# Optimization experiments

Hardware: AMD Instinct MI355X
Metric: run time of the kernel (lower is better)

## Reference

```python
import jax, jax.numpy as jnp
import numpy as np

N_HEADS = 16
HEAD_SIZE = 64
D_EMBD = 1024
BLOCK_SIZE = 1024
B, T = 4, 1024


def setup_inputs() -> dict:
    key = jax.random.key(0)
    ks = jax.random.split(key, 6)
    s = 0.02
    x = jax.random.normal(ks[0], (B, T, D_EMBD), dtype=jnp.float32)
    # per-head bias-free Q/K/V projections, stacked: [H, C, Hs]
    Wq = jax.random.normal(ks[1], (N_HEADS, D_EMBD, HEAD_SIZE), dtype=jnp.float32) * s
    Wk = jax.random.normal(ks[2], (N_HEADS, D_EMBD, HEAD_SIZE), dtype=jnp.float32) * s
    Wv = jax.random.normal(ks[3], (N_HEADS, D_EMBD, HEAD_SIZE), dtype=jnp.float32) * s
    # output projection W_o: Linear(d_embd, d_embd) with bias
    Wo = jax.random.normal(ks[4], (D_EMBD, D_EMBD), dtype=jnp.float32) * s
    bo = jax.random.normal(ks[5], (D_EMBD,), dtype=jnp.float32) * s
    return {"x": x, "Wq": Wq, "Wk": Wk, "Wv": Wv, "Wo": Wo, "bo": bo}


def reference(x, Wq, Wk, Wv, Wo, bo):
    # Batched equivalent of the per-head loop: q,k,v: [B, H, T, Hs]
    q = jnp.einsum('btc,hcs->bhts', x, Wq)
    k = jnp.einsum('btc,hcs->bhts', x, Wk)
    v = jnp.einsum('btc,hcs->bhts', x, Wv)
    scale = 1.0 / jnp.sqrt(jnp.asarray(HEAD_SIZE, dtype=x.dtype))
    scores = jnp.einsum('bhts,bhus->bhtu', q, k) * scale  # [B,H,T,T]
    causal = jnp.tril(jnp.ones((T, T), dtype=bool))
    scores = jnp.where(causal[None, None, :, :], scores, jnp.asarray(-jnp.inf, dtype=x.dtype))
    wei = jax.nn.softmax(scores, axis=-1)  # dropout p=0.0 -> identity
    out = jnp.einsum('bhtu,bhus->bhts', wei, v)  # [B,H,T,Hs]
    out = out.transpose(0, 2, 1, 3).reshape(B, T, D_EMBD)  # concat heads
    return out @ Wo.T + bo  # final Linear; dropout p=0.0 -> identity
```

## Files before the change

kernel.cpp:

```cpp
#include <hip/hip_runtime.h>
#include <hip/hip_bf16.h>
#include <math.h>

#define NH 16
#define HS 64
#define DE 1024
#define TT 1024
#define BBATCH 4
#define MTOK 4096

typedef __bf16 v8bf __attribute__((ext_vector_type(8)));
typedef __bf16 v4bf __attribute__((ext_vector_type(4)));
typedef float  v4f  __attribute__((ext_vector_type(4)));

__device__ __forceinline__ void gl_lds16(const __bf16* g, __bf16* l) {
    __builtin_amdgcn_global_load_lds(
        (const __attribute__((address_space(1))) unsigned int*)g,
        (__attribute__((address_space(3))) unsigned int*)l, 16, 0, 0);
}

__global__ __launch_bounds__(256) void prep_all_kernel(
    const float* __restrict__ x,  __bf16* __restrict__ xb,
    const float* __restrict__ Wo, __bf16* __restrict__ Wob,
    const float* __restrict__ Wq, const float* __restrict__ Wk,
    const float* __restrict__ Wv, __bf16* __restrict__ Wt)
{
    const int bid = blockIdx.x;
    const int t = threadIdx.x;
    if (bid < 5120) {
        int i = bid * 256 + t;
        const float* in; __bf16* out;
        if (i < 1048576) { in = x;  out = xb; }
        else             { in = Wo; out = Wob; i -= 1048576; }
        float4 v = ((const float4*)in)[i];
        v4bf o;
        o[0] = (__bf16)v.x; o[1] = (__bf16)v.y; o[2] = (__bf16)v.z; o[3] = (__bf16)v.w;
        *(v4bf*)&out[(size_t)i * 4] = o;
        return;
    }
    const int bid2 = bid - 5120;
    const int c0 = (bid2 & 15) * 64, h = (bid2 >> 4) & 15, m = bid2 >> 8;
    const float* W = (m == 0) ? Wq : (m == 1) ? Wk : Wv;
    __shared__ float tile[64][65];
    #pragma unroll
    for (int pp = 0; pp < 16; ++pp) {
        int cl = pp * 4 + (t >> 6);
        int s  = t & 63;
        tile[cl][s] = W[((size_t)h * DE + c0 + cl) * HS + s];
    }
    __syncthreads();
    #pragma unroll
    for (int pp = 0; pp < 16; ++pp) {
        int s  = pp * 4 + (t >> 6);
        int cl = t & 63;
        Wt[((size_t)(m * DE + h * HS + s)) * DE + c0 + cl] = (__bf16)tile[cl][s];
    }
}

__device__ __forceinline__ void gemm_stage(
    const __bf16* __restrict__ Ab, const __bf16* __restrict__ Bb,
    __bf16* As, __bf16* Bs, int K, int k0, int w, int l)
{
    #pragma unroll
    for (int i = 0; i < 4; ++i) {
        int p   = i * 256 + w * 64 + l;
        int row = p >> 3;
        int lc  = (p & 7) ^ (row & 7);
        gl_lds16(Ab + (size_t)row * K + k0 + lc * 8, As + p * 8);
        gl_lds16(Bb + (size_t)row * K + k0 + lc * 8, Bs + p * 8);
    }
}

__global__ __launch_bounds__(256) void gemm_bt_kernel(
    const __bf16* __restrict__ A, const __bf16* __restrict__ Bt,
    int K, int mode,
    __bf16* __restrict__ qk_out, __bf16* __restrict__ vt_out,
    float* __restrict__ f_out, const float* __restrict__ bias)
{
    __shared__ __align__(16) __bf16 As[2][128 * 64];
    __shared__ __align__(16) __bf16 Bs[2][128 * 64];
    const int tid = threadIdx.x;
    const int w = tid >> 6, l = tid & 63;
    const int wm = w >> 1, wn = w & 1;
    const int lhi = l >> 4, llo = l & 15;
    const int sw0 = ((lhi ^ (llo & 7)) << 3);
    const int sw1 = sw0 ^ 32;

    const int lin = blockIdx.x;
    const int xcd = lin & 7, j = lin >> 3;
    const int bm = xcd * 4 + (j & 3);
    const int bn = j >> 2;

    v4f acc[4][4];
    #pragma unroll
    for (int i = 0; i < 4; ++i)
        #pragma unroll
        for (int jj = 0; jj < 4; ++jj)
            #pragma unroll
            for (int r = 0; r < 4; ++r) acc[i][jj][r] = 0.f;

    const __bf16* Ab = A  + (size_t)bm * 128 * K;
    const __bf16* Bb = Bt + (size_t)bn * 128 * K;

    const int niter = K >> 6;
    gemm_stage(Ab, Bb, As[0], Bs[0], K, 0, w, l);

    for (int it = 0; it < niter; ++it) {
        const int buf = it & 1;
        __syncthreads();
        if (it + 1 < niter)
            gemm_stage(Ab, Bb, As[buf ^ 1], Bs[buf ^ 1], K, (it + 1) * 64, w, l);
        #pragma unroll
        for (int kk = 0; kk < 64; kk += 32) {
            const int sw = kk ? sw1 : sw0;
            v8bf a[4], b[4];
            #pragma unroll
            for (int i = 0; i < 4; ++i)
                a[i] = *(const v8bf*)&As[buf][(wm * 64 + i * 16 + llo) * 64 + sw];
            #pragma unroll
            for (int jj = 0; jj < 4; ++jj)
                b[jj] = *(const v8bf*)&Bs[buf][(wn * 64 + jj * 16 + llo) * 64 + sw];
            #pragma unroll
            for (int i = 0; i < 4; ++i)
                #pragma unroll
                for (int jj = 0; jj < 4; ++jj)
                    acc[i][jj] = __builtin_amdgcn_mfma_f32_16x16x32_bf16(a[i], b[jj], acc[i][jj], 0, 0, 0);
        }
    }

    const int row0 = bm * 128 + wm * 64;
    const int col0 = bn * 128 + wn * 64;

    if (mode == 0) {
        if (col0 < 2048) {
            #pragma unroll
            for (int i = 0; i < 4; ++i) {
                int rbase = row0 + i * 16 + lhi * 4;
                #pragma unroll
                for (int jj = 0; jj < 4; ++jj) {
                    int c = col0 + jj * 16 + llo;
                    #pragma unroll
                    for (int r = 0; r < 4; ++r)
                        qk_out[(size_t)(rbase + r) * 2048 + c] = (__bf16)acc[i][jj][r];
                }
            }
        } else {
            #pragma unroll
            for (int i = 0; i < 4; ++i) {
                int rbase = row0 + i * 16 + lhi * 4;
                int bidx = rbase >> 10, t0 = rbase & 1023;
                #pragma unroll
                for (int jj = 0; jj < 4; ++jj) {
                    int c = col0 + jj * 16 + llo - 2048;
                    v4bf pk;
                    #pragma unroll
                    for (int r = 0; r < 4; ++r) pk[r] = (__bf16)acc[i][jj][r];
                    *(v4bf*)&vt_out[((size_t)(bidx * NH + (c >> 6)) * HS + (c & 63)) * TT + t0] = pk;
                }
            }
        }
    } else {
        #pragma unroll
        for (int jj = 0; jj < 4; ++jj) {
            int c = col0 + jj * 16 + llo;
            float bv = bias[c];
            #pragma unroll
            for (int i = 0; i < 4; ++i) {
                int rbase = row0 + i * 16 + lhi * 4;
                #pragma unroll
                for (int r = 0; r < 4; ++r)
                    f_out[(size_t)(rbase + r) * DE + c] = acc[i][jj][r] + bv;
            }
        }
    }
}

__device__ __forceinline__ v4f bf_mfma(v8bf a, v8bf b, v4f c) {
    return __builtin_amdgcn_mfma_f32_16x16x32_bf16(a, b, c, 0, 0, 0);
}

__device__ __forceinline__ void stage_kv(
    const __bf16* __restrict__ kb, const __bf16* __restrict__ vb,
    __bf16* Ksb, __bf16* Vsb, int k0, int tid)
{
    #pragma unroll
    for (int i = 0; i < 2; ++i) {
        int p   = i * 256 + tid;
        int row = p >> 3;
        int lc  = (p & 7) ^ (row & 7);
        gl_lds16(kb + (size_t)(k0 + row) * 2048 + lc * 8, Ksb + p * 8);
        gl_lds16(vb + (size_t)row * TT + k0 + lc * 8,     Vsb + p * 8);
    }
}

template<bool DIAG>
__device__ __forceinline__ void attn_compute(
    const __bf16* __restrict__ Ksb, const __bf16* __restrict__ Vsb,
    __bf16* __restrict__ PsW, int k0, int r0, int lhi, int llo, int sw0, int sw1,
    v8bf aq0, v8bf aq1, v4f (&o)[4], float (&l_part)[4])
{
    v4f sacc[4];
    #pragma unroll
    for (int n = 0; n < 4; ++n)
        #pragma unroll
        for (int r = 0; r < 4; ++r) sacc[n][r] = 0.f;
    #pragma unroll
    for (int n = 0; n < 4; ++n) {
        v8bf bk0 = *(const v8bf*)&Ksb[(n * 16 + llo) * 64 + sw0];
        v8bf bk1 = *(const v8bf*)&Ksb[(n * 16 + llo) * 64 + sw1];
        sacc[n] = bf_mfma(aq0, bk0, sacc[n]);
        sacc[n] = bf_mfma(aq1, bk1, sacc[n]);
    }

    float prob[4][4];
    #pragma unroll
    for (int n = 0; n < 4; ++n) {
        int colg = k0 + n * 16 + llo;
        #pragma unroll
        for (int r = 0; r < 4; ++r) {
            float s2 = sacc[n][r] * 0.18033688f;
            if (DIAG) { int rowg = r0 + lhi * 4 + r; if (colg > rowg) s2 = -1e30f; }
            float p = exp2f(s2);
            prob[n][r] = p;
            l_part[r] += p;
        }
    }

    #pragma unroll
    for (int r = 0; r < 4; ++r)
        #pragma unroll
        for (int n = 0; n < 4; ++n)
            PsW[(lhi * 4 + r) * 72 + n * 16 + llo] = (__bf16)prob[n][r];

    #pragma unroll
    for (int kk = 0; kk < 64; kk += 32) {
        v8bf ap = *(const v8bf*)&PsW[llo * 72 + kk + lhi * 8];
        const int sw = kk ? sw1 : sw0;
        #pragma unroll
        for (int n = 0; n < 4; ++n) {
            v8bf bv = *(const v8bf*)&Vsb[(n * 16 + llo) * 64 + sw];
            o[n] = bf_mfma(ap, bv, o[n]);
        }
    }
}

__global__ __launch_bounds__(256) void attn_kernel(
    const __bf16* __restrict__ qk, const __bf16* __restrict__ vt,
    __bf16* __restrict__ att)
{
    __shared__ __align__(16) __bf16 Ks[2][64 * 64];
    __shared__ __align__(16) __bf16 Vs[2][64 * 64];
    __shared__ __align__(16) __bf16 Ps[4][16 * 72];

    const int tid = threadIdx.x;
    const int w = tid >> 6, l = tid & 63;
    const int lhi = l >> 4, llo = l & 15;
    const int sw0 = ((lhi ^ (llo & 7)) << 3);
    const int sw1 = sw0 ^ 32;
    const int bh = blockIdx.x & 63;
    const int qt = 15 - (blockIdx.x >> 6);
    const int b = bh >> 4, h = bh & 15;

    const __bf16* qbase = qk + (size_t)b * TT * 2048 + h * HS;
    const __bf16* kbase = qk + (size_t)b * TT * 2048 + 1024 + h * HS;
    const __bf16* vbase = vt + (size_t)bh * HS * TT;
    __bf16* PsW = &Ps[w][0];

    const int r0 = qt * 64 + w * 16;

    stage_kv(kbase, vbase, Ks[0], Vs[0], 0, tid);

    v8bf aq0 = *(const v8bf*)&qbase[(size_t)(r0 + llo) * 2048 + lhi * 8];
    v8bf aq1 = *(const v8bf*)&qbase[(size_t)(r0 + llo) * 2048 + 32 + lhi * 8];

    float l_part[4] = {0.f, 0.f, 0.f, 0.f};
    v4f o[4];
    #pragma unroll
    for (int n = 0; n < 4; ++n)
        #pragma unroll
        for (int r = 0; r < 4; ++r) o[n][r] = 0.f;

    for (int kt = 0; kt < qt; ++kt) {
        const int buf = kt & 1;
        __syncthreads();
        stage_kv(kbase, vbase, Ks[buf ^ 1], Vs[buf ^ 1], (kt + 1) * 64, tid);
        attn_compute<false>(Ks[buf], Vs[buf], PsW, kt * 64, r0, lhi, llo, sw0, sw1, aq0, aq1, o, l_part);
    }
    __syncthreads();
    attn_compute<true>(Ks[qt & 1], Vs[qt & 1], PsW, qt * 64, r0, lhi, llo, sw0, sw1, aq0, aq1, o, l_part);

    #pragma unroll
    for (int r = 0; r < 4; ++r) {
        float s = l_part[r];
        #pragma unroll
        for (int msk = 1; msk < 16; msk <<= 1) s += __shfl_xor(s, msk, 64);
        float inv = 1.f / s;
        int rowg = b * TT + r0 + lhi * 4 + r;
        #pragma unroll
        for (int n = 0; n < 4; ++n)
            att[(size_t)rowg * DE + h * HS + n * 16 + llo] = (__bf16)(o[n][r] * inv);
    }
}

extern "C" void kernel_launch(void* const* d_in, const int* in_sizes, int n_in,
                              void* d_out, int out_size, void* d_ws, size_t ws_size,
                              hipStream_t stream)
{
    const float* x  = (const float*)d_in[0];
    const float* Wq = (const float*)d_in[1];
    const float* Wk = (const float*)d_in[2];
    const float* Wv = (const float*)d_in[3];
    const float* Wo = (const float*)d_in[4];
    const float* bo = (const float*)d_in[5];
    float* out = (float*)d_out;

    char* ws = (char*)d_ws;
    __bf16* xb  = (__bf16*)(ws);
    __bf16* Wt  = (__bf16*)(ws + 8388608);
    __bf16* Wob = (__bf16*)(ws + 14680064);
    __bf16* qk  = (__bf16*)(ws + 16777216);
    __bf16* vt  = (__bf16*)(ws + 33554432);
    __bf16* att = (__bf16*)(ws + 41943040);

    prep_all_kernel<<<5888, 256, 0, stream>>>(x, xb, Wo, Wob, Wq, Wk, Wv, Wt);
    gemm_bt_kernel<<<768, 256, 0, stream>>>(xb, Wt, 1024, 0, qk, vt, nullptr, nullptr);
    attn_kernel<<<1024, 256, 0, stream>>>(qk, vt, att);
    gemm_bt_kernel<<<256, 256, 0, stream>>>(att, Wob, 1024, 1, nullptr, nullptr, out, bo);
}
```

Before: 167.8 us.

## Use 32x32x16 MFMA in attention with 128-row query tiles

Rewrites the attention kernel so each wave handles 32 query rows using 32x32x16 bf16 MFMA instead of 16x16x32, and each block covers 128 query rows, which halves the grid. Each staged K/V tile is reused across twice as many queries, and the larger MFMA shape reduces LDS reads per flop. In exchange, register use per thread rises (two 16-wide accumulators plus scores), the diagonal tiles do more masked wasted work, and fewer blocks may leave parallelism and load balance worse.

```diff
diff --git a/kernel.cpp b/kernel.cpp
--- a/kernel.cpp
+++ b/kernel.cpp
@@ -12,6 +12,7 @@
 typedef __bf16 v8bf __attribute__((ext_vector_type(8)));
 typedef __bf16 v4bf __attribute__((ext_vector_type(4)));
 typedef float  v4f  __attribute__((ext_vector_type(4)));
+typedef float  v16f __attribute__((ext_vector_type(16)));
 
 __device__ __forceinline__ void gl_lds16(const __bf16* g, __bf16* l) {
     __builtin_amdgcn_global_load_lds(
@@ -175,8 +176,8 @@
     }
 }
 
-__device__ __forceinline__ v4f bf_mfma(v8bf a, v8bf b, v4f c) {
-    return __builtin_amdgcn_mfma_f32_16x16x32_bf16(a, b, c, 0, 0, 0);
+__device__ __forceinline__ v16f bf_mfma32(v8bf a, v8bf b, v16f c) {
+    return __builtin_amdgcn_mfma_f32_32x32x16_bf16(a, b, c, 0, 0, 0);
 }
 
 __device__ __forceinline__ void stage_kv(
@@ -193,112 +194,105 @@
     }
 }
 
-template<bool DIAG>
-__device__ __forceinline__ void attn_compute(
-    const __bf16* __restrict__ Ksb, const __bf16* __restrict__ Vsb,
-    __bf16* __restrict__ PsW, int k0, int r0, int lhi, int llo, int sw0, int sw1,
-    v8bf aq0, v8bf aq1, v4f (&o)[4], float (&l_part)[4])
-{
-    v4f sacc[4];
-    #pragma unroll
-    for (int n = 0; n < 4; ++n)
-        #pragma unroll
-        for (int r = 0; r < 4; ++r) sacc[n][r] = 0.f;
-    #pragma unroll
-    for (int n = 0; n < 4; ++n) {
-        v8bf bk0 = *(const v8bf*)&Ksb[(n * 16 + llo) * 64 + sw0];
-        v8bf bk1 = *(const v8bf*)&Ksb[(n * 16 + llo) * 64 + sw1];
-        sacc[n] = bf_mfma(aq0, bk0, sacc[n]);
-        sacc[n] = bf_mfma(aq1, bk1, sacc[n]);
-    }
-
-    float prob[4][4];
-    #pragma unroll
-    for (int n = 0; n < 4; ++n) {
-        int colg = k0 + n * 16 + llo;
-        #pragma unroll
-        for (int r = 0; r < 4; ++r) {
-            float s2 = sacc[n][r] * 0.18033688f;
-            if (DIAG) { int rowg = r0 + lhi * 4 + r; if (colg > rowg) s2 = -1e30f; }
-            float p = exp2f(s2);
-            prob[n][r] = p;
-            l_part[r] += p;
-        }
-    }
-
-    #pragma unroll
-    for (int r = 0; r < 4; ++r)
-        #pragma unroll
-        for (int n = 0; n < 4; ++n)
-            PsW[(lhi * 4 + r) * 72 + n * 16 + llo] = (__bf16)prob[n][r];
-
-    #pragma unroll
-    for (int kk = 0; kk < 64; kk += 32) {
-        v8bf ap = *(const v8bf*)&PsW[llo * 72 + kk + lhi * 8];
-        const int sw = kk ? sw1 : sw0;
-        #pragma unroll
-        for (int n = 0; n < 4; ++n) {
-            v8bf bv = *(const v8bf*)&Vsb[(n * 16 + llo) * 64 + sw];
-            o[n] = bf_mfma(ap, bv, o[n]);
-        }
-    }
-}
-
 __global__ __launch_bounds__(256) void attn_kernel(
     const __bf16* __restrict__ qk, const __bf16* __restrict__ vt,
     __bf16* __restrict__ att)
 {
     __shared__ __align__(16) __bf16 Ks[2][64 * 64];
     __shared__ __align__(16) __bf16 Vs[2][64 * 64];
-    __shared__ __align__(16) __bf16 Ps[4][16 * 72];
+    __shared__ __align__(16) __bf16 Ps[4][32 * 72];
 
     const int tid = threadIdx.x;
     const int w = tid >> 6, l = tid & 63;
-    const int lhi = l >> 4, llo = l & 15;
-    const int sw0 = ((lhi ^ (llo & 7)) << 3);
-    const int sw1 = sw0 ^ 32;
+    const int m = l & 31, hh = l >> 5;
     const int bh = blockIdx.x & 63;
-    const int qt = 15 - (blockIdx.x >> 6);
-    const int b = bh >> 4, h = bh & 15;
-
-    const __bf16* qbase = qk + (size_t)b * TT * 2048 + h * HS;
-    const __bf16* kbase = qk + (size_t)b * TT * 2048 + 1024 + h * HS;
+    const int st = 7 - (blockIdx.x >> 6);
+    const int b = bh >> 4, hd = bh & 15;
+
+    const __bf16* qbase = qk + (size_t)b * TT * 2048 + hd * HS;
+    const __bf16* kbase = qk + (size_t)b * TT * 2048 + 1024 + hd * HS;
     const __bf16* vbase = vt + (size_t)bh * HS * TT;
     __bf16* PsW = &Ps[w][0];
 
-    const int r0 = qt * 64 + w * 16;
+    const int r0 = st * 128 + w * 32;
+
+    int offs[4];
+    #pragma unroll
+    for (int s = 0; s < 4; ++s) offs[s] = (((2 * s + hh) ^ (m & 7)) << 3);
 
     stage_kv(kbase, vbase, Ks[0], Vs[0], 0, tid);
 
-    v8bf aq0 = *(const v8bf*)&qbase[(size_t)(r0 + llo) * 2048 + lhi * 8];
-    v8bf aq1 = *(const v8bf*)&qbase[(size_t)(r0 + llo) * 2048 + 32 + lhi * 8];
-
-    float l_part[4] = {0.f, 0.f, 0.f, 0.f};
-    v4f o[4];
-    #pragma unroll
-    for (int n = 0; n < 4; ++n)
-        #pragma unroll
-        for (int r = 0; r < 4; ++r) o[n][r] = 0.f;
-
-    for (int kt = 0; kt < qt; ++kt) {
+    v8bf aq[4];
+    #pragma unroll
+    for (int s = 0; s < 4; ++s)
+        aq[s] = *(const v8bf*)&qbase[(size_t)(r0 + m) * 2048 + s * 16 + hh * 8];
+
+    float l_part[16];
+    #pragma unroll
+    for (int r = 0; r < 16; ++r) l_part[r] = 0.f;
+    v16f o0, o1;
+    #pragma unroll
+    for (int r = 0; r < 16; ++r) { o0[r] = 0.f; o1[r] = 0.f; }
+
+    const int ntiles = 2 * st + 2;
+    for (int kt = 0; kt < ntiles; ++kt) {
         const int buf = kt & 1;
+        const int k0 = kt * 64;
         __syncthreads();
-        stage_kv(kbase, vbase, Ks[buf ^ 1], Vs[buf ^ 1], (kt + 1) * 64, tid);
-        attn_compute<false>(Ks[buf], Vs[buf], PsW, kt * 64, r0, lhi, llo, sw0, sw1, aq0, aq1, o, l_part);
-    }
-    __syncthreads();
-    attn_compute<true>(Ks[qt & 1], Vs[qt & 1], PsW, qt * 64, r0, lhi, llo, sw0, sw1, aq0, aq1, o, l_part);
-
-    #pragma unroll
-    for (int r = 0; r < 4; ++r) {
+        if (kt + 1 < ntiles)
+            stage_kv(kbase, vbase, Ks[buf ^ 1], Vs[buf ^ 1], (kt + 1) * 64, tid);
+
+        const __bf16* Ksb = Ks[buf];
+        const __bf16* Vsb = Vs[buf];
+
+        v16f s0, s1;
+        #pragma unroll
+        for (int r = 0; r < 16; ++r) { s0[r] = 0.f; s1[r] = 0.f; }
+        #pragma unroll
+        for (int s = 0; s < 4; ++s) {
+            v8bf bk0 = *(const v8bf*)&Ksb[m * 64 + offs[s]];
+            v8bf bk1 = *(const v8bf*)&Ksb[(32 + m) * 64 + offs[s]];
+            s0 = bf_mfma32(aq[s], bk0, s0);
+            s1 = bf_mfma32(aq[s], bk1, s1);
+        }
+
+        const bool diag = (kt >= 2 * st);
+        #pragma unroll
+        for (int r = 0; r < 16; ++r) {
+            int row  = (r & 3) + 8 * (r >> 2) + 4 * hh;
+            int rowg = r0 + row;
+            float a0 = s0[r] * 0.18033688f;
+            float a1 = s1[r] * 0.18033688f;
+            if (diag) {
+                if (k0 + m > rowg)      a0 = -1e30f;
+                if (k0 + 32 + m > rowg) a1 = -1e30f;
+            }
+            float p0 = exp2f(a0), p1 = exp2f(a1);
+            l_part[r] += p0 + p1;
+            PsW[row * 72 + m]      = (__bf16)p0;
+            PsW[row * 72 + 32 + m] = (__bf16)p1;
+        }
+
+        #pragma unroll
+        for (int s = 0; s < 4; ++s) {
+            v8bf ap  = *(const v8bf*)&PsW[m * 72 + s * 16 + hh * 8];
+            v8bf bv0 = *(const v8bf*)&Vsb[m * 64 + offs[s]];
+            v8bf bv1 = *(const v8bf*)&Vsb[(32 + m) * 64 + offs[s]];
+            o0 = bf_mfma32(ap, bv0, o0);
+            o1 = bf_mfma32(ap, bv1, o1);
+        }
+    }
+
+    #pragma unroll
+    for (int r = 0; r < 16; ++r) {
         float s = l_part[r];
         #pragma unroll
-        for (int msk = 1; msk < 16; msk <<= 1) s += __shfl_xor(s, msk, 64);
+        for (int msk = 1; msk < 32; msk <<= 1) s += __shfl_xor(s, msk, 64);
         float inv = 1.f / s;
-        int rowg = b * TT + r0 + lhi * 4 + r;
-        #pragma unroll
-        for (int n = 0; n < 4; ++n)
-            att[(size_t)rowg * DE + h * HS + n * 16 + llo] = (__bf16)(o[n][r] * inv);
+        int row = (r & 3) + 8 * (r >> 2) + 4 * hh;
+        size_t rowg = (size_t)(b * TT + r0 + row);
+        att[rowg * DE + hd * HS + m]      = (__bf16)(o0[r] * inv);
+        att[rowg * DE + hd * HS + 32 + m] = (__bf16)(o1[r] * inv);
     }
 }
 
@@ -324,6 +318,6 @@
 
     prep_all_kernel<<<5888, 256, 0, stream>>>(x, xb, Wo, Wob, Wq, Wk, Wv, Wt);
     gemm_bt_kernel<<<768, 256, 0, stream>>>(xb, Wt, 1024, 0, qk, vt, nullptr, nullptr);
-    attn_kernel<<<1024, 256, 0, stream>>>(qk, vt, att);
+    attn_kernel<<<512, 256, 0, stream>>>(qk, vt, att);
     gemm_bt_kernel<<<256, 256, 0, stream>>>(att, Wob, 1024, 1, nullptr, nullptr, out, bo);
 }
```

Result: slower. 180.9 us (+7.8%).
